# Kernel optimization log

Measured on AMD Instinct MI355X. Metric: run time of the kernel, lower is better.

## Reference

```python
import jax, jax.numpy as jnp
import numpy as np

DELTA_VAR = 0.5
DELTA_DIST = 1.5
ALPHA = 1.0
BETA = 1.0
GAMMA = 0.001
NUM_INST = 32  # instance ids are 1..NUM_INST; 0 = background


def setup_inputs() -> dict:
    key = jax.random.key(0)
    k1, k2 = jax.random.split(key)
    embeddings = jax.random.normal(k1, (4, 16, 512, 512), dtype=jnp.float32)
    instance_labels = jax.random.randint(k2, (4, 512, 512), 0, NUM_INST + 1, dtype=jnp.int32)
    return {"embeddings": embeddings, "instance_labels": instance_labels}


def reference(embeddings, instance_labels):
    B, E, H, W = embeddings.shape
    HW = H * W
    S = NUM_INST + 1  # segment slots per batch incl. background slot 0

    emb = embeddings.transpose(0, 2, 3, 1).reshape(B, HW, E)   # [B, HW, E]
    lab = instance_labels.reshape(B, HW)                        # [B, HW]

    # ---- per-(batch, instance) means via one segment reduction ----
    seg = (jnp.arange(B, dtype=lab.dtype)[:, None] * S + lab).reshape(-1)
    sums = jax.ops.segment_sum(emb.reshape(-1, E), seg, num_segments=B * S).reshape(B, S, E)
    counts = jax.ops.segment_sum(jnp.ones((B * HW,), emb.dtype), seg, num_segments=B * S).reshape(B, S)
    means = sums / jnp.maximum(counts, 1.0)[..., None]          # [B, S, E]

    present = counts[:, 1:] > 0                                  # [B, K] instances only
    n = present.sum(-1).astype(emb.dtype)                        # [B] num_instances
    n_safe = jnp.maximum(n, 1.0)

    # ---- variance (pull) term: hinge(||e - mean||_2 - delta_var) ----
    mean_per_pix = jnp.take_along_axis(means, lab[:, :, None], axis=1)  # [B, HW, E]
    diff = emb - mean_per_pix
    pix_dist = jnp.sqrt(jnp.sum(diff * diff, axis=-1))           # [B, HW] (norm=2)
    hinge = jnp.maximum(pix_dist - DELTA_VAR, 0.0) * (lab > 0).astype(emb.dtype)
    var_loss = hinge.sum(-1) / n_safe                            # [B]

    # ---- distance (push) term: pairwise hinge(2*delta_dist - ||mi - mj||) ----
    m = means[:, 1:]                                             # [B, K, E]
    d2 = jnp.sum((m[:, :, None, :] - m[:, None, :, :]) ** 2, -1)  # [B, K, K]
    upper = jnp.triu(jnp.ones((NUM_INST, NUM_INST), bool), 1)
    pair_mask = upper[None] & present[:, :, None] & present[:, None, :]
    d = jnp.sqrt(jnp.where(pair_mask, d2, 1.0))
    pair_hinge = jnp.where(pair_mask, jnp.maximum(2.0 * DELTA_DIST - d, 0.0), 0.0)
    num_pairs = n * (n - 1.0) / 2.0
    dist_loss = jnp.where(n > 1, pair_hinge.sum((-1, -2)) / jnp.maximum(num_pairs, 1.0), 0.0)  # [B]

    # ---- regularization term: ||mean||_2 averaged over instances ----
    mnorm = jnp.sqrt(jnp.where(present, jnp.sum(m * m, -1), 1.0))
    reg_loss = jnp.where(present, mnorm, 0.0).sum(-1) / n_safe   # [B]

    total = ALPHA * var_loss.mean() + BETA * dist_loss.mean() + GAMMA * reg_loss.mean()
    return total
```

## Files before the change

kernel.cpp:

```cpp
#include <hip/hip_runtime.h>

#define NB 4
#define NE 16
#define NHW (512*512)
#define NINST 32
#define DELTA_VAR 0.5f
#define DELTA_DIST 1.5f
#define ALPHA 1.0f
#define BETA 1.0f
#define GAMMA 0.001f

typedef __attribute__((ext_vector_type(8))) short short8;
typedef __attribute__((ext_vector_type(4))) float f32x4;

#define PH_STRIDE 544
#define GRID_H 256
#define P_HIST 0
#define T_MEAN (GRID_H*PH_STRIDE)
#define T_MEAN_SZ (33*16)
#define T_DIST (T_MEAN + NB*T_MEAN_SZ)
#define T_REG  (T_DIST + NB)
#define T_NS   (T_REG + NB)
#define V_PART (T_NS + NB)

#define BLK_H 512
#define BPB_H (GRID_H/NB)
#define PXB_H 4096
#define PXW_H 512
#define CHUNKS_H 16
#define GRID_V 1024
#define BLK_V 256
#define BPB_V (GRID_V/NB)

#define LMREP 4
#define LMSTR 668

__device__ __forceinline__ unsigned f2bf(float x) {
    unsigned u = __builtin_bit_cast(unsigned, x);
    return (u + 0x7FFFu + ((u >> 16) & 1u)) >> 16;
}

__device__ __forceinline__ float wave_sum(float v) {
    #pragma unroll
    for (int o = 32; o > 0; o >>= 1) v += __shfl_down(v, o, 64);
    return v;
}

union PK { unsigned u[4]; short8 s; };

__global__ __launch_bounds__(BLK_H) void k_hist(const float* __restrict__ emb,
        const int* __restrict__ lab, float* __restrict__ ws) {
    __shared__ float red[8][2*NE][17];
    __shared__ float redc[8][2*NE];
    const int t = threadIdx.x;
    const int lane = t & 63;
    const int wv = t >> 6;
    const int colg = lane >> 4;
    const int cm = lane & 15;
    const int b = blockIdx.x / BPB_H;
    const int blk = blockIdx.x % BPB_H;

    const float* ebase = emb + (size_t)b*(NE*NHW) + (size_t)cm*NHW;
    const int* lbase = lab + (size_t)b*NHW;

    f32x4 acc_s0 = {0.f,0.f,0.f,0.f}, acc_s1 = {0.f,0.f,0.f,0.f};
    f32x4 acc_c0 = {0.f,0.f,0.f,0.f}, acc_c1 = {0.f,0.f,0.f,0.f};
    PK ones; ones.u[0]=ones.u[1]=ones.u[2]=ones.u[3]=0x3F803F80u;

    const int base = blk*PXB_H + wv*PXW_H;
    #pragma unroll 4
    for (int it = 0; it < CHUNKS_H; ++it) {
        const int ko = base + it*32 + colg*8;
        const float4 v0 = *(const float4*)(ebase + ko);
        const float4 v1 = *(const float4*)(ebase + ko + 4);
        const int4 L0 = *(const int4*)(lbase + ko);
        const int4 L1 = *(const int4*)(lbase + ko + 4);
        PK bf;
        bf.u[0] = f2bf(v0.x) | (f2bf(v0.y) << 16);
        bf.u[1] = f2bf(v0.z) | (f2bf(v0.w) << 16);
        bf.u[2] = f2bf(v1.x) | (f2bf(v1.y) << 16);
        bf.u[3] = f2bf(v1.z) | (f2bf(v1.w) << 16);
        const int la[8] = {L0.x,L0.y,L0.z,L0.w,L1.x,L1.y,L1.z,L1.w};
        PK a0, a1;
        #pragma unroll
        for (int p = 0; p < 4; ++p) {
            const unsigned lo0 = (la[2*p]   == cm+1 ) ? 0x3F80u : 0u;
            const unsigned hi0 = (la[2*p+1] == cm+1 ) ? 0x3F80u : 0u;
            const unsigned lo1 = (la[2*p]   == cm+17) ? 0x3F80u : 0u;
            const unsigned hi1 = (la[2*p+1] == cm+17) ? 0x3F80u : 0u;
            a0.u[p] = lo0 | (hi0 << 16);
            a1.u[p] = lo1 | (hi1 << 16);
        }
        acc_s0 = __builtin_amdgcn_mfma_f32_16x16x32_bf16(a0.s, bf.s,   acc_s0, 0,0,0);
        acc_s1 = __builtin_amdgcn_mfma_f32_16x16x32_bf16(a1.s, bf.s,   acc_s1, 0,0,0);
        acc_c0 = __builtin_amdgcn_mfma_f32_16x16x32_bf16(a0.s, ones.s, acc_c0, 0,0,0);
        acc_c1 = __builtin_amdgcn_mfma_f32_16x16x32_bf16(a1.s, ones.s, acc_c1, 0,0,0);
    }
    #pragma unroll
    for (int r = 0; r < 4; ++r) {
        red[wv][colg*4 + r][cm]      = acc_s0[r];
        red[wv][16 + colg*4 + r][cm] = acc_s1[r];
    }
    if (cm == 0) {
        #pragma unroll
        for (int r = 0; r < 4; ++r) {
            redc[wv][colg*4 + r]      = acc_c0[r];
            redc[wv][16 + colg*4 + r] = acc_c1[r];
        }
    }
    __syncthreads();
    float* dst = ws + P_HIST + (size_t)blockIdx.x*PH_STRIDE;
    for (int i = t; i < PH_STRIDE; i += BLK_H) {
        float v;
        if (i < 512) {
            const int s = i >> 4, e = i & 15;
            v = red[0][s][e]+red[1][s][e]+red[2][s][e]+red[3][s][e]
              + red[4][s][e]+red[5][s][e]+red[6][s][e]+red[7][s][e];
        } else {
            const int s = i - 512;
            v = redc[0][s]+redc[1][s]+redc[2][s]+redc[3][s]
              + redc[4][s]+redc[5][s]+redc[6][s]+redc[7][s];
        }
        dst[i] = v;
    }
}

__global__ void k_stats(float* __restrict__ ws) {
    const int b = blockIdx.x;
    const int t = threadIdx.x;
    __shared__ float lred[PH_STRIDE];
    __shared__ float lmean[NINST*17];
    __shared__ float lcnt[NINST];
    __shared__ int lpres[NINST];
    const float* ph = ws + P_HIST + (size_t)(b*BPB_H)*PH_STRIDE;
    for (int i = t; i < PH_STRIDE; i += 256) {
        float s = 0.f;
        #pragma unroll 8
        for (int k = 0; k < BPB_H; k++) s += ph[(size_t)k*PH_STRIDE + i];
        lred[i] = s;
    }
    __syncthreads();
    if (t < NINST) {
        const float c = lred[512 + t];
        lcnt[t] = c;
        lpres[t] = (c > 0.f) ? 1 : 0;
    }
    __syncthreads();
    for (int i = t; i < 512; i += 256) {
        const int s = i >> 4, e = i & 15;
        lmean[s*17 + e] = lred[i] / fmaxf(lcnt[s], 1.f);
    }
    __syncthreads();
    for (int i = t; i < 33*NE; i += 256) {
        const int l = i >> 4, e = i & 15;
        ws[T_MEAN + b*T_MEAN_SZ + i] = (l == 0) ? 0.f : lmean[(l-1)*17 + e];
    }
    if (t < 64) {
        const int lane = t;
        const int n = __popcll(__ballot((lane < NINST) ? (lpres[lane] != 0) : false));
        float dsum = 0.f;
        for (int idx = lane; idx < NINST*NINST; idx += 64) {
            const int i = idx >> 5, j = idx & 31;
            if (i < j && lpres[i] && lpres[j]) {
                float d2 = 0.f;
                #pragma unroll
                for (int e = 0; e < NE; e++) {
                    const float df = lmean[i*17+e] - lmean[j*17+e];
                    d2 += df*df;
                }
                dsum += fmaxf(2.f*DELTA_DIST - sqrtf(d2), 0.f);
            }
        }
        dsum = wave_sum(dsum);
        float rsum = 0.f;
        if (lane < NINST && lpres[lane]) {
            float s2 = 0.f;
            #pragma unroll
            for (int e = 0; e < NE; e++) { const float m = lmean[lane*17+e]; s2 += m*m; }
            rsum = sqrtf(s2);
        }
        rsum = wave_sum(rsum);
        if (lane == 0) {
            const float nf = (float)n;
            const float nsafe = fmaxf(nf, 1.f);
            ws[T_DIST+b] = (n > 1) ? dsum / fmaxf(nf*(nf-1.f)*0.5f, 1.f) : 0.f;
            ws[T_REG+b] = rsum / nsafe;
            ws[T_NS+b] = nsafe;
        }
    }
}

__global__ __launch_bounds__(BLK_V) void k_var(const float* __restrict__ emb,
        const int* __restrict__ lab, float* __restrict__ ws) {
    __shared__ __align__(16) float lm[LMREP*LMSTR];
    __shared__ float wred[4];
    const int t = threadIdx.x;
    const int b = blockIdx.x >> 8;
    const int blk = blockIdx.x & 255;
    for (int c4 = 0; c4 < LMREP; ++c4) {
        for (int i = t; i < 33*20; i += BLK_V) {
            const int l = i / 20, e = i % 20;
            if (e < 16) lm[c4*LMSTR + i] = ws[T_MEAN + b*T_MEAN_SZ + l*16 + e];
        }
    }
    __syncthreads();
    const float* lmc = lm + ((t >> 4) & (LMREP-1))*LMSTR;
    const float* ebase = emb + (size_t)b*(NE*NHW);
    const int* lbase = lab + (size_t)b*NHW;

    const int p = (blk*BLK_V + t)*4;
    const int4 l4 = *(const int4*)(lbase + p);
    float4 m0[4], m1[4], m2[4], m3[4];
    {
        const float4* q0 = (const float4*)(lmc + l4.x*20);
        const float4* q1 = (const float4*)(lmc + l4.y*20);
        const float4* q2 = (const float4*)(lmc + l4.z*20);
        const float4* q3 = (const float4*)(lmc + l4.w*20);
        #pragma unroll
        for (int c = 0; c < 4; ++c) { m0[c]=q0[c]; m1[c]=q1[c]; m2[c]=q2[c]; m3[c]=q3[c]; }
    }
    float d0=0.f, d1=0.f, d2=0.f, d3=0.f;
    #pragma unroll
    for (int e = 0; e < NE; e++) {
        const float4 v = *(const float4*)(ebase + (size_t)e*NHW + p);
        float df;
        df = v.x - ((const float*)&m0[e>>2])[e&3]; d0 += df*df;
        df = v.y - ((const float*)&m1[e>>2])[e&3]; d1 += df*df;
        df = v.z - ((const float*)&m2[e>>2])[e&3]; d2 += df*df;
        df = v.w - ((const float*)&m3[e>>2])[e&3]; d3 += df*df;
    }
    float acc = 0.f;
    if (l4.x > 0) acc += fmaxf(sqrtf(d0) - DELTA_VAR, 0.f);
    if (l4.y > 0) acc += fmaxf(sqrtf(d1) - DELTA_VAR, 0.f);
    if (l4.z > 0) acc += fmaxf(sqrtf(d2) - DELTA_VAR, 0.f);
    if (l4.w > 0) acc += fmaxf(sqrtf(d3) - DELTA_VAR, 0.f);

    const float wsum = wave_sum(acc);
    if ((t & 63) == 0) wred[t >> 6] = wsum;
    __syncthreads();
    if (t == 0) ws[V_PART + blockIdx.x] = wred[0]+wred[1]+wred[2]+wred[3];
}

__global__ void k_final(const float* __restrict__ ws, float* __restrict__ out) {
    const int t = threadIdx.x;
    __shared__ float vb[4];
    float s = 0.f;
    #pragma unroll
    for (int k = 0; k < 4; ++k) s += ws[V_PART + t*4 + k];
    s = wave_sum(s);
    if ((t & 63) == 0) vb[t >> 6] = s;
    __syncthreads();
    if (t == 0) {
        float tot = 0.f;
        for (int b = 0; b < NB; b++) {
            tot += ALPHA * (vb[b] / ws[T_NS+b])
                 + BETA * ws[T_DIST+b]
                 + GAMMA * ws[T_REG+b];
        }
        out[0] = tot * (1.f/NB);
    }
}

extern "C" void kernel_launch(void* const* d_in, const int* in_sizes, int n_in,
                              void* d_out, int out_size, void* d_ws, size_t ws_size,
                              hipStream_t stream) {
    const float* emb = (const float*)d_in[0];
    const int* lab = (const int*)d_in[1];
    float* out = (float*)d_out;
    float* ws = (float*)d_ws;

    k_hist<<<GRID_H, BLK_H, 0, stream>>>(emb, lab, ws);
    k_stats<<<NB, 256, 0, stream>>>(ws);
    k_var<<<GRID_V, BLK_V, 0, stream>>>(emb, lab, ws);
    k_final<<<1, 256, 0, stream>>>(ws, out);
}
```

Before: 53.46 us.

## Fold final reduction into k_var via atomics, retile hist, transpose partials

Removes the k_final launch by having each k_var block atomically add its partial sum and the last block compute the total. k_hist moves from 256 blocks of 512 threads to 512 blocks of 256 threads, and writes its partial histograms transposed so k_stats can sum them with float4 loads. k_var now issues all embedding loads before staging the means into LDS, which overlaps global latency with the LDS fill. The atomic float accumulation makes the summation order nondeterministic, and the counter reset depends on k_stats running first.

```diff
diff --git a/kernel.cpp b/kernel.cpp
--- a/kernel.cpp
+++ b/kernel.cpp
@@ -13,27 +13,27 @@
 typedef __attribute__((ext_vector_type(8))) short short8;
 typedef __attribute__((ext_vector_type(4))) float f32x4;
 
+#define GRID_H 512
+#define BLK_H 256
+#define BPB_H (GRID_H/NB)
+#define PXB_H (NHW/BPB_H)
+#define CHUNKS_H 16
 #define PH_STRIDE 544
-#define GRID_H 256
+
+#define GRID_V 1024
+#define BLK_V 256
+
 #define P_HIST 0
 #define T_MEAN (GRID_H*PH_STRIDE)
-#define T_MEAN_SZ (33*16)
+#define T_MEAN_SZ (33*NE)
 #define T_DIST (T_MEAN + NB*T_MEAN_SZ)
 #define T_REG  (T_DIST + NB)
 #define T_NS   (T_REG + NB)
-#define V_PART (T_NS + NB)
-
-#define BLK_H 512
-#define BPB_H (GRID_H/NB)
-#define PXB_H 4096
-#define PXW_H 512
-#define CHUNKS_H 16
-#define GRID_V 1024
-#define BLK_V 256
-#define BPB_V (GRID_V/NB)
+#define VACC   (T_NS + NB)
+#define VCNT   (VACC + NB)
 
 #define LMREP 4
-#define LMSTR 668
+#define LMSTR 660
 
 __device__ __forceinline__ unsigned f2bf(float x) {
     unsigned u = __builtin_bit_cast(unsigned, x);
@@ -50,8 +50,8 @@
 
 __global__ __launch_bounds__(BLK_H) void k_hist(const float* __restrict__ emb,
         const int* __restrict__ lab, float* __restrict__ ws) {
-    __shared__ float red[8][2*NE][17];
-    __shared__ float redc[8][2*NE];
+    __shared__ float red[4][2*NE][17];
+    __shared__ float redc[4][2*NE];
     const int t = threadIdx.x;
     const int lane = t & 63;
     const int wv = t >> 6;
@@ -67,7 +67,7 @@
     f32x4 acc_c0 = {0.f,0.f,0.f,0.f}, acc_c1 = {0.f,0.f,0.f,0.f};
     PK ones; ones.u[0]=ones.u[1]=ones.u[2]=ones.u[3]=0x3F803F80u;
 
-    const int base = blk*PXB_H + wv*PXW_H;
+    const int base = blk*PXB_H + wv*(PXB_H/4);
     #pragma unroll 4
     for (int it = 0; it < CHUNKS_H; ++it) {
         const int ko = base + it*32 + colg*8;
@@ -109,19 +109,17 @@
         }
     }
     __syncthreads();
-    float* dst = ws + P_HIST + (size_t)blockIdx.x*PH_STRIDE;
+    float* dst = ws + P_HIST + (size_t)b*PH_STRIDE*BPB_H + blk;
     for (int i = t; i < PH_STRIDE; i += BLK_H) {
         float v;
         if (i < 512) {
             const int s = i >> 4, e = i & 15;
-            v = red[0][s][e]+red[1][s][e]+red[2][s][e]+red[3][s][e]
-              + red[4][s][e]+red[5][s][e]+red[6][s][e]+red[7][s][e];
+            v = red[0][s][e] + red[1][s][e] + red[2][s][e] + red[3][s][e];
         } else {
             const int s = i - 512;
-            v = redc[0][s]+redc[1][s]+redc[2][s]+redc[3][s]
-              + redc[4][s]+redc[5][s]+redc[6][s]+redc[7][s];
-        }
-        dst[i] = v;
+            v = redc[0][s] + redc[1][s] + redc[2][s] + redc[3][s];
+        }
+        dst[(size_t)i*BPB_H] = v;
     }
 }
 
@@ -132,18 +130,26 @@
     __shared__ float lmean[NINST*17];
     __shared__ float lcnt[NINST];
     __shared__ int lpres[NINST];
-    const float* ph = ws + P_HIST + (size_t)(b*BPB_H)*PH_STRIDE;
+    const float* ph = ws + P_HIST + (size_t)b*PH_STRIDE*BPB_H;
     for (int i = t; i < PH_STRIDE; i += 256) {
-        float s = 0.f;
+        const float4* r4 = (const float4*)(ph + (size_t)i*BPB_H);
+        float4 s4 = {0.f,0.f,0.f,0.f};
         #pragma unroll 8
-        for (int k = 0; k < BPB_H; k++) s += ph[(size_t)k*PH_STRIDE + i];
-        lred[i] = s;
+        for (int k = 0; k < BPB_H/4; k++) {
+            const float4 v = r4[k];
+            s4.x += v.x; s4.y += v.y; s4.z += v.z; s4.w += v.w;
+        }
+        lred[i] = s4.x + s4.y + s4.z + s4.w;
     }
     __syncthreads();
     if (t < NINST) {
         const float c = lred[512 + t];
         lcnt[t] = c;
         lpres[t] = (c > 0.f) ? 1 : 0;
+    }
+    if (t == 0) {
+        ws[VACC + b] = 0.f;
+        if (b == 0) ((unsigned*)ws)[VCNT] = 0u;
     }
     __syncthreads();
     for (int i = t; i < 512; i += 256) {
@@ -191,43 +197,50 @@
 }
 
 __global__ __launch_bounds__(BLK_V) void k_var(const float* __restrict__ emb,
-        const int* __restrict__ lab, float* __restrict__ ws) {
+        const int* __restrict__ lab, float* __restrict__ ws, float* __restrict__ out) {
     __shared__ __align__(16) float lm[LMREP*LMSTR];
     __shared__ float wred[4];
     const int t = threadIdx.x;
     const int b = blockIdx.x >> 8;
     const int blk = blockIdx.x & 255;
-    for (int c4 = 0; c4 < LMREP; ++c4) {
-        for (int i = t; i < 33*20; i += BLK_V) {
-            const int l = i / 20, e = i % 20;
-            if (e < 16) lm[c4*LMSTR + i] = ws[T_MEAN + b*T_MEAN_SZ + l*16 + e];
-        }
-    }
-    __syncthreads();
-    const float* lmc = lm + ((t >> 4) & (LMREP-1))*LMSTR;
     const float* ebase = emb + (size_t)b*(NE*NHW);
     const int* lbase = lab + (size_t)b*NHW;
-
     const int p = (blk*BLK_V + t)*4;
+
     const int4 l4 = *(const int4*)(lbase + p);
-    float4 m0[4], m1[4], m2[4], m3[4];
-    {
-        const float4* q0 = (const float4*)(lmc + l4.x*20);
-        const float4* q1 = (const float4*)(lmc + l4.y*20);
-        const float4* q2 = (const float4*)(lmc + l4.z*20);
-        const float4* q3 = (const float4*)(lmc + l4.w*20);
-        #pragma unroll
-        for (int c = 0; c < 4; ++c) { m0[c]=q0[c]; m1[c]=q1[c]; m2[c]=q2[c]; m3[c]=q3[c]; }
-    }
+    float4 ev[NE];
+    #pragma unroll
+    for (int e = 0; e < NE; e++) ev[e] = *(const float4*)(ebase + (size_t)e*NHW + p);
+
+    for (int i = t; i < 33*NE; i += BLK_V) {
+        const int l = i >> 4, e = i & 15;
+        const float v = ws[T_MEAN + b*T_MEAN_SZ + i];
+        #pragma unroll
+        for (int r = 0; r < LMREP; r++) lm[r*LMSTR + l*20 + e] = v;
+    }
+    __syncthreads();
+
+    const float* lmc = lm + ((t >> 4) & (LMREP-1))*LMSTR;
+    const float4* q0 = (const float4*)(lmc + l4.x*20);
+    const float4* q1 = (const float4*)(lmc + l4.y*20);
+    const float4* q2 = (const float4*)(lmc + l4.z*20);
+    const float4* q3 = (const float4*)(lmc + l4.w*20);
     float d0=0.f, d1=0.f, d2=0.f, d3=0.f;
     #pragma unroll
-    for (int e = 0; e < NE; e++) {
-        const float4 v = *(const float4*)(ebase + (size_t)e*NHW + p);
-        float df;
-        df = v.x - ((const float*)&m0[e>>2])[e&3]; d0 += df*df;
-        df = v.y - ((const float*)&m1[e>>2])[e&3]; d1 += df*df;
-        df = v.z - ((const float*)&m2[e>>2])[e&3]; d2 += df*df;
-        df = v.w - ((const float*)&m3[e>>2])[e&3]; d3 += df*df;
+    for (int c = 0; c < 4; c++) {
+        const float4 ma = q0[c];
+        const float4 mb = q1[c];
+        const float4 mc_ = q2[c];
+        const float4 md = q3[c];
+        #pragma unroll
+        for (int j = 0; j < 4; j++) {
+            const float4 v = ev[4*c + j];
+            float df;
+            df = v.x - ((const float*)&ma)[j];  d0 += df*df;
+            df = v.y - ((const float*)&mb)[j];  d1 += df*df;
+            df = v.z - ((const float*)&mc_)[j]; d2 += df*df;
+            df = v.w - ((const float*)&md)[j];  d3 += df*df;
+        }
     }
     float acc = 0.f;
     if (l4.x > 0) acc += fmaxf(sqrtf(d0) - DELTA_VAR, 0.f);
@@ -238,26 +251,21 @@
     const float wsum = wave_sum(acc);
     if ((t & 63) == 0) wred[t >> 6] = wsum;
     __syncthreads();
-    if (t == 0) ws[V_PART + blockIdx.x] = wred[0]+wred[1]+wred[2]+wred[3];
-}
-
-__global__ void k_final(const float* __restrict__ ws, float* __restrict__ out) {
-    const int t = threadIdx.x;
-    __shared__ float vb[4];
-    float s = 0.f;
-    #pragma unroll
-    for (int k = 0; k < 4; ++k) s += ws[V_PART + t*4 + k];
-    s = wave_sum(s);
-    if ((t & 63) == 0) vb[t >> 6] = s;
-    __syncthreads();
     if (t == 0) {
-        float tot = 0.f;
-        for (int b = 0; b < NB; b++) {
-            tot += ALPHA * (vb[b] / ws[T_NS+b])
-                 + BETA * ws[T_DIST+b]
-                 + GAMMA * ws[T_REG+b];
-        }
-        out[0] = tot * (1.f/NB);
+        atomicAdd(&ws[VACC + b], wred[0]+wred[1]+wred[2]+wred[3]);
+        __threadfence();
+        const unsigned old = atomicAdd((unsigned*)&ws[VCNT], 1u);
+        if (old == GRID_V - 1) {
+            float tot = 0.f;
+            #pragma unroll
+            for (int bb = 0; bb < NB; bb++) {
+                const float v = atomicAdd(&ws[VACC + bb], 0.f);
+                tot += ALPHA * (v / ws[T_NS+bb])
+                     + BETA * ws[T_DIST+bb]
+                     + GAMMA * ws[T_REG+bb];
+            }
+            out[0] = tot * (1.f/NB);
+        }
     }
 }
 
@@ -271,6 +279,5 @@
 
     k_hist<<<GRID_H, BLK_H, 0, stream>>>(emb, lab, ws);
     k_stats<<<NB, 256, 0, stream>>>(ws);
-    k_var<<<GRID_V, BLK_V, 0, stream>>>(emb, lab, ws);
-    k_final<<<1, 256, 0, stream>>>(ws, out);
-}
+    k_var<<<GRID_V, BLK_V, 0, stream>>>(emb, lab, ws, out);
+}
```

New measurement: 78.26 us. 1.46x slower.
